# Optimization experiments

Measured on AMD Instinct MI355X. Metric: run time of the kernel, lower is better.

## Reference

```python
import jax, jax.numpy as jnp
import numpy as np

N_NODES = 20000
N_EDGES = 640000
D = 128            # node feature dim
NUM_HEADS = 4      # = num_irreps of edge_sh (lmax=3, 0e+1o+2e+3o)
HEAD_DIM = D // NUM_HEADS
IR_DIMS = np.array([1, 3, 5, 7])  # dims of each irrep; sum = 16
AVG_NUM_NEIGHBORS = 32.0


def setup_inputs() -> dict:
    key = jax.random.key(0)
    ks = jax.random.split(key, 20)
    inp = {
        "edge_sh": jax.random.normal(ks[0], (N_EDGES, int(IR_DIMS.sum())), jnp.float32),
        "node_feats": jax.random.normal(ks[1], (N_NODES, D), jnp.float32),
        "edge_feats": jax.random.normal(ks[2], (N_EDGES, 64), jnp.float32),
        "chi_scalar": jax.random.normal(ks[3], (N_EDGES, 64), jnp.float32),
        "cutoffs": jax.random.uniform(ks[4], (N_EDGES,), jnp.float32),
        "senders": jax.random.randint(ks[5], (N_EDGES,), 0, N_NODES),
        "receivers": jax.random.randint(ks[6], (N_EDGES,), 0, N_NODES),
        # radial MLP: 64 -> 128 -> 128 (silu between)
        "W_rad1": jax.random.normal(ks[7], (64, 128), jnp.float32) / np.sqrt(64),
        "b_rad1": jnp.zeros((128,), jnp.float32),
        "W_rad2": jax.random.normal(ks[8], (128, 128), jnp.float32) / np.sqrt(128),
        "b_rad2": jnp.zeros((128,), jnp.float32),
        # spherical-scalar MLP: 64 -> 128 -> 128
        "W_sph1": jax.random.normal(ks[9], (64, 128), jnp.float32) / np.sqrt(64),
        "b_sph1": jnp.zeros((128,), jnp.float32),
        "W_sph2": jax.random.normal(ks[10], (128, 128), jnp.float32) / np.sqrt(128),
        "b_sph2": jnp.zeros((128,), jnp.float32),
        # Q/K projections, no bias
        "Wq": jax.random.normal(ks[11], (D, D), jnp.float32) / np.sqrt(D),
        "Wk": jax.random.normal(ks[12], (D, D), jnp.float32) / np.sqrt(D),
    }
    return inp


def reference(edge_sh, node_feats, edge_feats, chi_scalar, cutoffs, senders,
              receivers, W_rad1, b_rad1, W_rad2, b_rad2, W_sph1, b_sph1,
              W_sph2, b_sph2, Wq, Wk):
    silu = jax.nn.silu
    # edge filter: radial MLP + spherical-scalar MLP
    w = silu(edge_feats @ W_rad1 + b_rad1) @ W_rad2 + b_rad2      # [E, D]
    w = w + (silu(chi_scalar @ W_sph1 + b_sph1) @ W_sph2 + b_sph2)
    w = w.reshape(-1, NUM_HEADS, HEAD_DIM)                        # [E, H, hd]
    # gathered queries/keys
    q = (node_feats @ Wq).reshape(-1, NUM_HEADS, HEAD_DIM)[receivers]
    k = (node_feats @ Wk).reshape(-1, NUM_HEADS, HEAD_DIM)[senders]
    # filter-scaled attention: per-edge, per-head scalar
    alpha = (q * w * k).sum(axis=-1) * (1.0 / np.sqrt(HEAD_DIM))  # [E, H]
    alpha = alpha * cutoffs[:, None]
    # aligned_mul: broadcast per-irrep weight over each irrep's dim (mul=1)
    y = jnp.repeat(alpha, IR_DIMS, axis=-1)                       # [E, 16]
    msg = edge_sh * y
    # scatter_sum into receivers
    chi = jax.ops.segment_sum(msg, receivers, num_segments=N_NODES)
    return chi / AVG_NUM_NEIGHBORS
```

## Files before the change

### kernel.cpp

```cpp
#include <hip/hip_runtime.h>
#include <cmath>

#define NNODES 20000
#define NEDGES 640000
#define DDIM   128
#define TN     16
#define BE     64

typedef __attribute__((ext_vector_type(8))) short bf16x8;
typedef __attribute__((ext_vector_type(4))) float f32x4;

__device__ __forceinline__ unsigned short f2bf(float x) {
    union { float f; unsigned u; } v; v.f = x;
    unsigned r = v.u + 0x7FFFu + ((v.u >> 16) & 1u);
    return (unsigned short)(r >> 16);
}

__device__ __forceinline__ unsigned cvtpk(float lo, float hi) {
    unsigned r;
    asm("v_cvt_pk_bf16_f32 %0, %1, %2" : "=v"(r) : "v"(lo), "v"(hi));
    return r;
}

__global__ void pack_weights(const float* __restrict__ W, unsigned short* __restrict__ dst)
{
    const int f  = blockIdx.x;
    const int kt = f >> 3, nt = f & 7;
    const int t  = threadIdx.x;
#pragma unroll
    for (int ii = 0; ii < 2; ii++) {
        const int idx  = t * 2 + ii;
        const int lane = idx >> 3, i = idx & 7;
        const int k = kt * 32 + (lane >> 4) * 8 + i;
        const int n = nt * 16 + (lane & 15);
        dst[f * 512 + idx] = f2bf(W[k * 128 + n]);
    }
}

__global__ __launch_bounds__(256) void qk_proj_kernel(
    const float* __restrict__ nf, const float* __restrict__ Wq,
    const float* __restrict__ Wk, float* __restrict__ qbuf,
    float* __restrict__ kbuf)
{
    __shared__ float s_nf[TN * DDIM];
    const int t  = threadIdx.x;
    const int n0 = blockIdx.x * TN;
    {
        const float4* src = (const float4*)(nf + (size_t)n0 * DDIM);
        float4* dst = (float4*)s_nf;
        for (int i = t; i < TN * DDIM / 4; i += 256) dst[i] = src[i];
    }
    __syncthreads();

    const int j = t & 127;
    const float* W = (t < 128) ? Wq : Wk;
    float acc[TN];
#pragma unroll
    for (int n = 0; n < TN; n++) acc[n] = 0.f;

    for (int k = 0; k < DDIM; k += 4) {
        const float w0 = W[(k + 0) * DDIM + j];
        const float w1 = W[(k + 1) * DDIM + j];
        const float w2 = W[(k + 2) * DDIM + j];
        const float w3 = W[(k + 3) * DDIM + j];
#pragma unroll
        for (int n = 0; n < TN; n++) {
            const float4 f = *(const float4*)&s_nf[n * DDIM + k];
            acc[n] = fmaf(f.w, w3, fmaf(f.z, w2, fmaf(f.y, w1, fmaf(f.x, w0, acc[n]))));
        }
    }
    float* outp = (t < 128) ? qbuf : kbuf;
    for (int n = 0; n < TN; n++) outp[(size_t)(n0 + n) * DDIM + j] = acc[n];
}

__global__ __launch_bounds__(256, 3) void edge_kernel(
    const float* __restrict__ edge_sh, const float* __restrict__ cutoffs,
    const int* __restrict__ senders, const int* __restrict__ receivers,
    const float* __restrict__ edge_feats, const float* __restrict__ chi_scalar,
    const unsigned short* __restrict__ w1r, const unsigned short* __restrict__ w1s,
    const unsigned short* __restrict__ w2r, const unsigned short* __restrict__ w2s,
    const float* __restrict__ b_rad1, const float* __restrict__ b_sph1,
    const float* __restrict__ b_rad2, const float* __restrict__ b_sph2,
    const float* __restrict__ qbuf, const float* __restrict__ kbuf,
    float* __restrict__ out)
{
    __shared__ unsigned short s_a[2 * 64 * 64];
    __shared__ unsigned short s_h[64 * 128];
    __shared__ float s_alpha[64][4];
    char* pa = (char*)s_a;
    char* ph = (char*)s_h;

    const int t  = threadIdx.x;
    const int w  = t >> 6;
    const int l  = t & 63;
    const int eb = blockIdx.x * BE;

    const int el     = l & 15;
    const int c0base = w * 32 + (l >> 4) * 4;
    f32x4 qk[2][4];
    float cut[4];
#pragma unroll
    for (int et = 0; et < 4; et++) {
        const int eg = eb + et * 16 + el;
        const int rn = receivers[eg];
        const int sn = senders[eg];
        cut[et] = cutoffs[eg];
#pragma unroll
        for (int ct = 0; ct < 2; ct++) {
            const int c0 = c0base + ct * 16;
            const float4 qv = *(const float4*)(qbuf + (size_t)rn * 128 + c0);
            const float4 kv = *(const float4*)(kbuf + (size_t)sn * 128 + c0);
            qk[ct][et] = (f32x4){ qv.x * kv.x, qv.y * kv.y, qv.z * kv.z, qv.w * kv.w };
        }
    }
    f32x4 b2s[2];
#pragma unroll
    for (int ct = 0; ct < 2; ct++) {
        const float4 br = *(const float4*)(b_rad2 + c0base + ct * 16);
        const float4 bs = *(const float4*)(b_sph2 + c0base + ct * 16);
        b2s[ct] = (f32x4){ br.x + bs.x, br.y + bs.y, br.z + bs.z, br.w + bs.w };
    }
#pragma unroll
    for (int ct = 0; ct < 2; ct++) {
#pragma unroll
        for (int et = 0; et < 4; et++)
            asm volatile("" : "+v"(qk[ct][et]));
        asm volatile("" : "+v"(b2s[ct]));
    }

#pragma unroll
    for (int ii = 0; ii < 4; ii++) {
        const int idx = t + ii * 256;
        const int r   = idx >> 4;
        const int c4  = idx & 15;
        const float4 a = *(const float4*)(edge_feats + (size_t)(eb + r) * 64 + c4 * 4);
        const float4 b = *(const float4*)(chi_scalar + (size_t)(eb + r) * 64 + c4 * 4);
        const uint2 av = { cvtpk(a.x, a.y), cvtpk(a.z, a.w) };
        const uint2 bv = { cvtpk(b.x, b.y), cvtpk(b.z, b.w) };
        const int off = (r * 128 + c4 * 8) ^ ((r & 7) << 4);
        *(uint2*)(pa + off)        = av;
        *(uint2*)(pa + 8192 + off) = bv;
    }
    __syncthreads();

    f32x4 acc2[2][4];
#pragma unroll
    for (int ct = 0; ct < 2; ct++)
#pragma unroll
        for (int et = 0; et < 4; et++)
            acc2[ct][et] = (f32x4){0.f, 0.f, 0.f, 0.f};

    for (int path = 0; path < 2; path++) {
        const unsigned short* W1p = path ? w1s : w1r;
        const unsigned short* W2p = path ? w2s : w2r;
        const float* b1p = path ? b_sph1 : b_rad1;
        const char*  ab  = pa + path * 8192;

        f32x4 acc1[2][4];
#pragma unroll
        for (int ht = 0; ht < 2; ht++)
#pragma unroll
            for (int et = 0; et < 4; et++)
                acc1[ht][et] = (f32x4){0.f, 0.f, 0.f, 0.f};

#pragma unroll
        for (int kt = 0; kt < 2; kt++) {
            bf16x8 bfrag[4];
#pragma unroll
            for (int et = 0; et < 4; et++) {
                const int e = et * 16 + (l & 15);
                const int k = kt * 32 + (l >> 4) * 8;
                bfrag[et] = *(const bf16x8*)(ab + ((e * 128 + k * 2) ^ ((e & 7) << 4)));
            }
#pragma unroll
            for (int ht = 0; ht < 2; ht++) {
                const int f = kt * 8 + (w * 2 + ht);
                const bf16x8 afrag = *(const bf16x8*)(W1p + (size_t)f * 512 + l * 8);
#pragma unroll
                for (int et = 0; et < 4; et++)
                    acc1[ht][et] = __builtin_amdgcn_mfma_f32_16x16x32_bf16(
                        afrag, bfrag[et], acc1[ht][et], 0, 0, 0);
            }
        }

#pragma unroll
        for (int ht = 0; ht < 2; ht++) {
            const int hid0 = w * 32 + ht * 16 + (l >> 4) * 4;
            const float4 bv = *(const float4*)(b1p + hid0);
            const float* bvf = (const float*)&bv;
#pragma unroll
            for (int et = 0; et < 4; et++) {
                const int e = et * 16 + (l & 15);
                float s[4];
#pragma unroll
                for (int r = 0; r < 4; r++) {
                    const float v = acc1[ht][et][r] + bvf[r];
                    s[r] = v * __builtin_amdgcn_rcpf(1.0f + __expf(-v));
                }
                const uint2 hv = { cvtpk(s[0], s[1]), cvtpk(s[2], s[3]) };
                *(uint2*)(ph + ((e * 256 + hid0 * 2) ^ ((e & 7) << 4))) = hv;
            }
        }
        __syncthreads();

#pragma unroll
        for (int kt = 0; kt < 4; kt++) {
            bf16x8 hfrag[4];
#pragma unroll
            for (int et = 0; et < 4; et++) {
                const int e = et * 16 + (l & 15);
                const int k = kt * 32 + (l >> 4) * 8;
                hfrag[et] = *(const bf16x8*)(ph + ((e * 256 + k * 2) ^ ((e & 7) << 4)));
            }
#pragma unroll
            for (int ct = 0; ct < 2; ct++) {
                const int f = kt * 8 + (w * 2 + ct);
                const bf16x8 afrag = *(const bf16x8*)(W2p + (size_t)f * 512 + l * 8);
#pragma unroll
                for (int et = 0; et < 4; et++)
                    acc2[ct][et] = __builtin_amdgcn_mfma_f32_16x16x32_bf16(
                        afrag, hfrag[et], acc2[ct][et], 0, 0, 0);
            }
        }
        if (path == 0) __syncthreads();
    }

#pragma unroll
    for (int et = 0; et < 4; et++) {
        float vsum = 0.f;
#pragma unroll
        for (int ct = 0; ct < 2; ct++) {
#pragma unroll
            for (int r = 0; r < 4; r++)
                vsum = fmaf(qk[ct][et][r], acc2[ct][et][r] + b2s[ct][r], vsum);
        }
        vsum += __shfl_xor(vsum, 16, 64);
        vsum += __shfl_xor(vsum, 32, 64);
        if (l < 16) {
            s_alpha[et * 16 + l][w] = vsum * cut[et] * 0.005524271728019903f;
        }
    }
    __syncthreads();

    {
        const int e   = t >> 2;
        const int c0q = t & 3;
        const int eg  = eb + e;
        const int rn  = receivers[eg];
        const float4 sh = *(const float4*)(edge_sh + (size_t)eg * 16 + c0q * 4);
        const float* shf = (const float*)&sh;
#pragma unroll
        for (int j = 0; j < 4; j++) {
            const int comp = c0q * 4 + j;
            const int head = (comp == 0) ? 0 : (comp < 4) ? 1 : (comp < 9) ? 2 : 3;
            atomicAdd(&out[(size_t)rn * 16 + comp], shf[j] * s_alpha[e][head]);
        }
    }
}

extern "C" void kernel_launch(void* const* d_in, const int* in_sizes, int n_in,
                              void* d_out, int out_size, void* d_ws, size_t ws_size,
                              hipStream_t stream)
{
    const float* edge_sh    = (const float*)d_in[0];
    const float* node_feats = (const float*)d_in[1];
    const float* edge_feats = (const float*)d_in[2];
    const float* chi_scalar = (const float*)d_in[3];
    const float* cutoffs    = (const float*)d_in[4];
    const int*   senders    = (const int*)d_in[5];
    const int*   receivers  = (const int*)d_in[6];
    const float* W_rad1 = (const float*)d_in[7];
    const float* b_rad1 = (const float*)d_in[8];
    const float* W_rad2 = (const float*)d_in[9];
    const float* b_rad2 = (const float*)d_in[10];
    const float* W_sph1 = (const float*)d_in[11];
    const float* b_sph1 = (const float*)d_in[12];
    const float* W_sph2 = (const float*)d_in[13];
    const float* b_sph2 = (const float*)d_in[14];
    const float* Wq     = (const float*)d_in[15];
    const float* Wk     = (const float*)d_in[16];

    float* out  = (float*)d_out;
    float* qbuf = (float*)d_ws;
    float* kbuf = qbuf + (size_t)NNODES * DDIM;
    unsigned short* w1r = (unsigned short*)(kbuf + (size_t)NNODES * DDIM);
    unsigned short* w1s = w1r + 16 * 512;
    unsigned short* w2r = w1s + 16 * 512;
    unsigned short* w2s = w2r + 32 * 512;

    hipMemsetAsync(out, 0, (size_t)out_size * sizeof(float), stream);

    pack_weights<<<16, 256, 0, stream>>>(W_rad1, w1r);
    pack_weights<<<16, 256, 0, stream>>>(W_sph1, w1s);
    pack_weights<<<32, 256, 0, stream>>>(W_rad2, w2r);
    pack_weights<<<32, 256, 0, stream>>>(W_sph2, w2s);

    qk_proj_kernel<<<NNODES / TN, 256, 0, stream>>>(node_feats, Wq, Wk, qbuf, kbuf);

    edge_kernel<<<NEDGES / BE, 256, 0, stream>>>(
        edge_sh, cutoffs, senders, receivers, edge_feats, chi_scalar,
        w1r, w1s, w2r, w2s, b_rad1, b_sph1, b_rad2, b_sph2,
        qbuf, kbuf, out);
}
```

Baseline: 360.7 us.

## Make edge kernel persistent with software-pipelined prefetch of next tile

Converts the edge kernel into a persistent grid of 512 blocks that loop over edge tiles. While the current tile's MLP runs, it prefetches the next tile's indices, q/k gathers and edge/chi features into registers, hiding global-memory latency behind the MFMA work. Occupancy drops to 2 blocks per CU, and register pressure rises because of the prefetch buffers. Barriers are replaced with a custom lgkmcnt wait plus s_barrier.

```diff
diff --git a/kernel.cpp b/kernel.cpp
--- a/kernel.cpp
+++ b/kernel.cpp
@@ -6,6 +6,8 @@
 #define DDIM   128
 #define TN     16
 #define BE     64
+#define NTILES (NEDGES / BE)
+#define NBLK   512
 
 typedef __attribute__((ext_vector_type(8))) short bf16x8;
 typedef __attribute__((ext_vector_type(4))) float f32x4;
@@ -15,11 +17,13 @@
     unsigned r = v.u + 0x7FFFu + ((v.u >> 16) & 1u);
     return (unsigned short)(r >> 16);
 }
-
 __device__ __forceinline__ unsigned cvtpk(float lo, float hi) {
     unsigned r;
     asm("v_cvt_pk_bf16_f32 %0, %1, %2" : "=v"(r) : "v"(lo), "v"(hi));
     return r;
+}
+__device__ __forceinline__ void BAR() {
+    asm volatile("s_waitcnt lgkmcnt(0)\n\ts_barrier" ::: "memory");
 }
 
 __global__ void pack_weights(const float* __restrict__ W, unsigned short* __restrict__ dst)
@@ -73,7 +77,7 @@
     for (int n = 0; n < TN; n++) outp[(size_t)(n0 + n) * DDIM + j] = acc[n];
 }
 
-__global__ __launch_bounds__(256, 3) void edge_kernel(
+__global__ __launch_bounds__(256, 2) void edge_kernel(
     const float* __restrict__ edge_sh, const float* __restrict__ cutoffs,
     const int* __restrict__ senders, const int* __restrict__ receivers,
     const float* __restrict__ edge_feats, const float* __restrict__ chi_scalar,
@@ -93,26 +97,11 @@
     const int t  = threadIdx.x;
     const int w  = t >> 6;
     const int l  = t & 63;
-    const int eb = blockIdx.x * BE;
-
-    const int el     = l & 15;
+    const int el = l & 15;
     const int c0base = w * 32 + (l >> 4) * 4;
-    f32x4 qk[2][4];
-    float cut[4];
-#pragma unroll
-    for (int et = 0; et < 4; et++) {
-        const int eg = eb + et * 16 + el;
-        const int rn = receivers[eg];
-        const int sn = senders[eg];
-        cut[et] = cutoffs[eg];
-#pragma unroll
-        for (int ct = 0; ct < 2; ct++) {
-            const int c0 = c0base + ct * 16;
-            const float4 qv = *(const float4*)(qbuf + (size_t)rn * 128 + c0);
-            const float4 kv = *(const float4*)(kbuf + (size_t)sn * 128 + c0);
-            qk[ct][et] = (f32x4){ qv.x * kv.x, qv.y * kv.y, qv.z * kv.z, qv.w * kv.w };
-        }
-    }
+
+    int tile = blockIdx.x;
+
     f32x4 b2s[2];
 #pragma unroll
     for (int ct = 0; ct < 2; ct++) {
@@ -120,141 +109,226 @@
         const float4 bs = *(const float4*)(b_sph2 + c0base + ct * 16);
         b2s[ct] = (f32x4){ br.x + bs.x, br.y + bs.y, br.z + bs.z, br.w + bs.w };
     }
-#pragma unroll
-    for (int ct = 0; ct < 2; ct++) {
+    float4 b1v[2][2];
+#pragma unroll
+    for (int ht = 0; ht < 2; ht++) {
+        const int hid0 = w * 32 + ht * 16 + (l >> 4) * 4;
+        b1v[0][ht] = *(const float4*)(b_rad1 + hid0);
+        b1v[1][ht] = *(const float4*)(b_sph1 + hid0);
+    }
+
+    float cutC[4], cutN[4], cutP[4];
+    int rnN[4], snN[4];
+    f32x4 qraw[2][4], kraw[2][4];
+    {
+        int rn0[4], sn0[4];
+#pragma unroll
+        for (int et = 0; et < 4; et++) {
+            const int eg = tile * BE + et * 16 + el;
+            rn0[et] = receivers[eg]; sn0[et] = senders[eg]; cutC[et] = cutoffs[eg];
+        }
 #pragma unroll
         for (int et = 0; et < 4; et++)
-            asm volatile("" : "+v"(qk[ct][et]));
-        asm volatile("" : "+v"(b2s[ct]));
-    }
-
-#pragma unroll
-    for (int ii = 0; ii < 4; ii++) {
-        const int idx = t + ii * 256;
-        const int r   = idx >> 4;
-        const int c4  = idx & 15;
-        const float4 a = *(const float4*)(edge_feats + (size_t)(eb + r) * 64 + c4 * 4);
-        const float4 b = *(const float4*)(chi_scalar + (size_t)(eb + r) * 64 + c4 * 4);
-        const uint2 av = { cvtpk(a.x, a.y), cvtpk(a.z, a.w) };
-        const uint2 bv = { cvtpk(b.x, b.y), cvtpk(b.z, b.w) };
-        const int off = (r * 128 + c4 * 8) ^ ((r & 7) << 4);
-        *(uint2*)(pa + off)        = av;
-        *(uint2*)(pa + 8192 + off) = bv;
-    }
-    __syncthreads();
-
-    f32x4 acc2[2][4];
+#pragma unroll
+            for (int ct = 0; ct < 2; ct++) {
+                const float4 qv = *(const float4*)(qbuf + (size_t)rn0[et] * 128 + c0base + ct * 16);
+                const float4 kv = *(const float4*)(kbuf + (size_t)sn0[et] * 128 + c0base + ct * 16);
+                qraw[ct][et] = (f32x4){ qv.x, qv.y, qv.z, qv.w };
+                kraw[ct][et] = (f32x4){ kv.x, kv.y, kv.z, kv.w };
+            }
+        if (tile + NBLK < NTILES) {
+#pragma unroll
+            for (int et = 0; et < 4; et++) {
+                const int eg = (tile + NBLK) * BE + et * 16 + el;
+                rnN[et] = receivers[eg]; snN[et] = senders[eg]; cutN[et] = cutoffs[eg];
+            }
+        }
+#pragma unroll
+        for (int ii = 0; ii < 4; ii++) {
+            const int idx = t + ii * 256;
+            const int r = idx >> 4, c4 = idx & 15;
+            const float4 a = *(const float4*)(edge_feats + (size_t)(tile * BE + r) * 64 + c4 * 4);
+            const float4 b = *(const float4*)(chi_scalar + (size_t)(tile * BE + r) * 64 + c4 * 4);
+            const uint2 av = { cvtpk(a.x, a.y), cvtpk(a.z, a.w) };
+            const uint2 bv = { cvtpk(b.x, b.y), cvtpk(b.z, b.w) };
+            const int off = (r * 128 + c4 * 8) ^ ((r & 7) << 4);
+            *(uint2*)(pa + off)        = av;
+            *(uint2*)(pa + 8192 + off) = bv;
+        }
+        BAR();
+    }
+    f32x4 prod[2][4];
 #pragma unroll
     for (int ct = 0; ct < 2; ct++)
 #pragma unroll
         for (int et = 0; et < 4; et++)
-            acc2[ct][et] = (f32x4){0.f, 0.f, 0.f, 0.f};
-
-    for (int path = 0; path < 2; path++) {
-        const unsigned short* W1p = path ? w1s : w1r;
-        const unsigned short* W2p = path ? w2s : w2r;
-        const float* b1p = path ? b_sph1 : b_rad1;
-        const char*  ab  = pa + path * 8192;
-
-        f32x4 acc1[2][4];
-#pragma unroll
-        for (int ht = 0; ht < 2; ht++)
+            prod[ct][et] = qraw[ct][et] * kraw[ct][et];
+
+    float4 efr[4], chr[4];
+
+    for (;;) {
+        const int next = tile + NBLK;
+        const bool have_next = (next < NTILES);
+
+        if (have_next) {
 #pragma unroll
             for (int et = 0; et < 4; et++)
-                acc1[ht][et] = (f32x4){0.f, 0.f, 0.f, 0.f};
-
-#pragma unroll
-        for (int kt = 0; kt < 2; kt++) {
-            bf16x8 bfrag[4];
+#pragma unroll
+                for (int ct = 0; ct < 2; ct++) {
+                    const float4 qv = *(const float4*)(qbuf + (size_t)rnN[et] * 128 + c0base + ct * 16);
+                    const float4 kv = *(const float4*)(kbuf + (size_t)snN[et] * 128 + c0base + ct * 16);
+                    qraw[ct][et] = (f32x4){ qv.x, qv.y, qv.z, qv.w };
+                    kraw[ct][et] = (f32x4){ kv.x, kv.y, kv.z, kv.w };
+                }
+        }
+#pragma unroll
+        for (int et = 0; et < 4; et++) cutP[et] = cutN[et];
+        if (next + NBLK < NTILES) {
 #pragma unroll
             for (int et = 0; et < 4; et++) {
-                const int e = et * 16 + (l & 15);
-                const int k = kt * 32 + (l >> 4) * 8;
-                bfrag[et] = *(const bf16x8*)(ab + ((e * 128 + k * 2) ^ ((e & 7) << 4)));
-            }
+                const int eg = (next + NBLK) * BE + et * 16 + el;
+                rnN[et] = receivers[eg]; snN[et] = senders[eg]; cutN[et] = cutoffs[eg];
+            }
+        }
+        const int se = tile * BE + (t >> 2);
+        const int rvS = receivers[se];
+        const float4 shS = *(const float4*)(edge_sh + (size_t)se * 16 + (t & 3) * 4);
+
+        f32x4 acc2[2][4];
+#pragma unroll
+        for (int ct = 0; ct < 2; ct++)
+#pragma unroll
+            for (int et = 0; et < 4; et++)
+                acc2[ct][et] = (f32x4){0.f, 0.f, 0.f, 0.f};
+
+#pragma unroll
+        for (int path = 0; path < 2; path++) {
+            const unsigned short* W1p = path ? w1s : w1r;
+            const unsigned short* W2p = path ? w2s : w2r;
+            const char* ab = pa + path * 8192;
+
+            f32x4 acc1[2][4];
+#pragma unroll
+            for (int ht = 0; ht < 2; ht++)
+#pragma unroll
+                for (int et = 0; et < 4; et++)
+                    acc1[ht][et] = (f32x4){0.f, 0.f, 0.f, 0.f};
+
+#pragma unroll
+            for (int kt = 0; kt < 2; kt++) {
+                bf16x8 bfrag[4];
+#pragma unroll
+                for (int et = 0; et < 4; et++) {
+                    const int e = et * 16 + el;
+                    const int k = kt * 32 + (l >> 4) * 8;
+                    bfrag[et] = *(const bf16x8*)(ab + ((e * 128 + k * 2) ^ ((e & 7) << 4)));
+                }
+#pragma unroll
+                for (int ht = 0; ht < 2; ht++) {
+                    const bf16x8 afrag = *(const bf16x8*)(W1p + (size_t)(kt * 8 + w * 2 + ht) * 512 + l * 8);
+#pragma unroll
+                    for (int et = 0; et < 4; et++)
+                        acc1[ht][et] = __builtin_amdgcn_mfma_f32_16x16x32_bf16(
+                            afrag, bfrag[et], acc1[ht][et], 0, 0, 0);
+                }
+            }
+
 #pragma unroll
             for (int ht = 0; ht < 2; ht++) {
-                const int f = kt * 8 + (w * 2 + ht);
-                const bf16x8 afrag = *(const bf16x8*)(W1p + (size_t)f * 512 + l * 8);
-#pragma unroll
-                for (int et = 0; et < 4; et++)
-                    acc1[ht][et] = __builtin_amdgcn_mfma_f32_16x16x32_bf16(
-                        afrag, bfrag[et], acc1[ht][et], 0, 0, 0);
-            }
-        }
-
-#pragma unroll
-        for (int ht = 0; ht < 2; ht++) {
-            const int hid0 = w * 32 + ht * 16 + (l >> 4) * 4;
-            const float4 bv = *(const float4*)(b1p + hid0);
-            const float* bvf = (const float*)&bv;
-#pragma unroll
-            for (int et = 0; et < 4; et++) {
-                const int e = et * 16 + (l & 15);
-                float s[4];
-#pragma unroll
-                for (int r = 0; r < 4; r++) {
-                    const float v = acc1[ht][et][r] + bvf[r];
-                    s[r] = v * __builtin_amdgcn_rcpf(1.0f + __expf(-v));
-                }
-                const uint2 hv = { cvtpk(s[0], s[1]), cvtpk(s[2], s[3]) };
-                *(uint2*)(ph + ((e * 256 + hid0 * 2) ^ ((e & 7) << 4))) = hv;
-            }
-        }
-        __syncthreads();
-
-#pragma unroll
-        for (int kt = 0; kt < 4; kt++) {
-            bf16x8 hfrag[4];
-#pragma unroll
-            for (int et = 0; et < 4; et++) {
-                const int e = et * 16 + (l & 15);
-                const int k = kt * 32 + (l >> 4) * 8;
-                hfrag[et] = *(const bf16x8*)(ph + ((e * 256 + k * 2) ^ ((e & 7) << 4)));
-            }
-#pragma unroll
-            for (int ct = 0; ct < 2; ct++) {
-                const int f = kt * 8 + (w * 2 + ct);
-                const bf16x8 afrag = *(const bf16x8*)(W2p + (size_t)f * 512 + l * 8);
-#pragma unroll
-                for (int et = 0; et < 4; et++)
-                    acc2[ct][et] = __builtin_amdgcn_mfma_f32_16x16x32_bf16(
-                        afrag, hfrag[et], acc2[ct][et], 0, 0, 0);
-            }
-        }
-        if (path == 0) __syncthreads();
-    }
-
-#pragma unroll
-    for (int et = 0; et < 4; et++) {
-        float vsum = 0.f;
-#pragma unroll
-        for (int ct = 0; ct < 2; ct++) {
-#pragma unroll
-            for (int r = 0; r < 4; r++)
-                vsum = fmaf(qk[ct][et][r], acc2[ct][et][r] + b2s[ct][r], vsum);
-        }
-        vsum += __shfl_xor(vsum, 16, 64);
-        vsum += __shfl_xor(vsum, 32, 64);
-        if (l < 16) {
-            s_alpha[et * 16 + l][w] = vsum * cut[et] * 0.005524271728019903f;
-        }
-    }
-    __syncthreads();
-
-    {
-        const int e   = t >> 2;
-        const int c0q = t & 3;
-        const int eg  = eb + e;
-        const int rn  = receivers[eg];
-        const float4 sh = *(const float4*)(edge_sh + (size_t)eg * 16 + c0q * 4);
-        const float* shf = (const float*)&sh;
-#pragma unroll
-        for (int j = 0; j < 4; j++) {
-            const int comp = c0q * 4 + j;
-            const int head = (comp == 0) ? 0 : (comp < 4) ? 1 : (comp < 9) ? 2 : 3;
-            atomicAdd(&out[(size_t)rn * 16 + comp], shf[j] * s_alpha[e][head]);
-        }
+                const int hid0 = w * 32 + ht * 16 + (l >> 4) * 4;
+                const float* bvf = (const float*)&b1v[path][ht];
+#pragma unroll
+                for (int et = 0; et < 4; et++) {
+                    const int e = et * 16 + el;
+                    float s[4];
+#pragma unroll
+                    for (int r = 0; r < 4; r++) {
+                        const float v = acc1[ht][et][r] + bvf[r];
+                        s[r] = v * __builtin_amdgcn_rcpf(1.0f + __expf(-v));
+                    }
+                    const uint2 hv = { cvtpk(s[0], s[1]), cvtpk(s[2], s[3]) };
+                    *(uint2*)(ph + ((e * 256 + hid0 * 2) ^ ((e & 7) << 4))) = hv;
+                }
+            }
+            BAR();
+
+#pragma unroll
+            for (int kt = 0; kt < 4; kt++) {
+                bf16x8 hfrag[4];
+#pragma unroll
+                for (int et = 0; et < 4; et++) {
+                    const int e = et * 16 + el;
+                    const int k = kt * 32 + (l >> 4) * 8;
+                    hfrag[et] = *(const bf16x8*)(ph + ((e * 256 + k * 2) ^ ((e & 7) << 4)));
+                }
+#pragma unroll
+                for (int ct = 0; ct < 2; ct++) {
+                    const bf16x8 afrag = *(const bf16x8*)(W2p + (size_t)(kt * 8 + w * 2 + ct) * 512 + l * 8);
+#pragma unroll
+                    for (int et = 0; et < 4; et++)
+                        acc2[ct][et] = __builtin_amdgcn_mfma_f32_16x16x32_bf16(
+                            afrag, hfrag[et], acc2[ct][et], 0, 0, 0);
+                }
+            }
+            if (path == 0) BAR();
+        }
+
+        if (have_next) {
+#pragma unroll
+            for (int ii = 0; ii < 4; ii++) {
+                const int idx = t + ii * 256;
+                const int r = idx >> 4, c4 = idx & 15;
+                efr[ii] = *(const float4*)(edge_feats + (size_t)(next * BE + r) * 64 + c4 * 4);
+                chr[ii] = *(const float4*)(chi_scalar + (size_t)(next * BE + r) * 64 + c4 * 4);
+            }
+        }
+#pragma unroll
+        for (int et = 0; et < 4; et++) {
+            float vsum = 0.f;
+#pragma unroll
+            for (int ct = 0; ct < 2; ct++)
+#pragma unroll
+                for (int r = 0; r < 4; r++)
+                    vsum = fmaf(prod[ct][et][r], acc2[ct][et][r] + b2s[ct][r], vsum);
+            vsum += __shfl_xor(vsum, 16, 64);
+            vsum += __shfl_xor(vsum, 32, 64);
+            if (l < 16) {
+                s_alpha[et * 16 + l][w] = vsum * cutC[et] * 0.005524271728019903f;
+            }
+        }
+        BAR();
+
+        {
+            const float* shf = (const float*)&shS;
+#pragma unroll
+            for (int j = 0; j < 4; j++) {
+                const int comp = (t & 3) * 4 + j;
+                const int head = (comp == 0) ? 0 : (comp < 4) ? 1 : (comp < 9) ? 2 : 3;
+                atomicAdd(&out[(size_t)rvS * 16 + comp], shf[j] * s_alpha[t >> 2][head]);
+            }
+        }
+
+        if (!have_next) break;
+
+#pragma unroll
+        for (int ct = 0; ct < 2; ct++)
+#pragma unroll
+            for (int et = 0; et < 4; et++)
+                prod[ct][et] = qraw[ct][et] * kraw[ct][et];
+#pragma unroll
+        for (int ii = 0; ii < 4; ii++) {
+            const int idx = t + ii * 256;
+            const int r = idx >> 4, c4 = idx & 15;
+            const uint2 av = { cvtpk(efr[ii].x, efr[ii].y), cvtpk(efr[ii].z, efr[ii].w) };
+            const uint2 bv = { cvtpk(chr[ii].x, chr[ii].y), cvtpk(chr[ii].z, chr[ii].w) };
+            const int off = (r * 128 + c4 * 8) ^ ((r & 7) << 4);
+            *(uint2*)(pa + off)        = av;
+            *(uint2*)(pa + 8192 + off) = bv;
+        }
+#pragma unroll
+        for (int et = 0; et < 4; et++) cutC[et] = cutP[et];
+        BAR();
+        tile = next;
     }
 }
 
@@ -297,7 +371,7 @@
 
     qk_proj_kernel<<<NNODES / TN, 256, 0, stream>>>(node_feats, Wq, Wk, qbuf, kbuf);
 
-    edge_kernel<<<NEDGES / BE, 256, 0, stream>>>(
+    edge_kernel<<<NBLK, 256, 0, stream>>>(
         edge_sh, cutoffs, senders, receivers, edge_feats, chi_scalar,
         w1r, w1s, w2r, w2s, b_rad1, b_sph1, b_rad2, b_sph2,
         qbuf, kbuf, out);
```

Result: slower. 712.8 us (+97.6%).

## Store Q/K in bf16 and stage q*k products in LDS instead of registers

Applied to the files above, without the earlier changes.

The Q/K projection now writes bf16 instead of fp32, which halves the bytes the edge kernel gathers per edge. The edge kernel computes q*k products with coalesced row-wise gathers, stores them as bf16 in a swizzled shared buffer, and reads them back after the MLP GEMMs rather than keeping them in registers. The launch-bounds occupancy hint is dropped and the path loop is unrolled. The change adds 16KB of LDS per block and extra rounding of q, k and their product to bf16, which lowers precision.

```diff
diff --git a/kernel.cpp b/kernel.cpp
--- a/kernel.cpp
+++ b/kernel.cpp
@@ -9,13 +9,16 @@
 
 typedef __attribute__((ext_vector_type(8))) short bf16x8;
 typedef __attribute__((ext_vector_type(4))) float f32x4;
+typedef __attribute__((ext_vector_type(4))) unsigned short us4;
 
 __device__ __forceinline__ unsigned short f2bf(float x) {
     union { float f; unsigned u; } v; v.f = x;
     unsigned r = v.u + 0x7FFFu + ((v.u >> 16) & 1u);
     return (unsigned short)(r >> 16);
 }
-
+__device__ __forceinline__ float bf2f(unsigned short h) {
+    union { unsigned u; float f; } v; v.u = ((unsigned)h) << 16; return v.f;
+}
 __device__ __forceinline__ unsigned cvtpk(float lo, float hi) {
     unsigned r;
     asm("v_cvt_pk_bf16_f32 %0, %1, %2" : "=v"(r) : "v"(lo), "v"(hi));
@@ -39,8 +42,8 @@
 
 __global__ __launch_bounds__(256) void qk_proj_kernel(
     const float* __restrict__ nf, const float* __restrict__ Wq,
-    const float* __restrict__ Wk, float* __restrict__ qbuf,
-    float* __restrict__ kbuf)
+    const float* __restrict__ Wk, unsigned short* __restrict__ qbuf,
+    unsigned short* __restrict__ kbuf)
 {
     __shared__ float s_nf[TN * DDIM];
     const int t  = threadIdx.x;
@@ -69,11 +72,11 @@
             acc[n] = fmaf(f.w, w3, fmaf(f.z, w2, fmaf(f.y, w1, fmaf(f.x, w0, acc[n]))));
         }
     }
-    float* outp = (t < 128) ? qbuf : kbuf;
-    for (int n = 0; n < TN; n++) outp[(size_t)(n0 + n) * DDIM + j] = acc[n];
-}
-
-__global__ __launch_bounds__(256, 3) void edge_kernel(
+    unsigned short* outp = (t < 128) ? qbuf : kbuf;
+    for (int n = 0; n < TN; n++) outp[(size_t)(n0 + n) * DDIM + j] = f2bf(acc[n]);
+}
+
+__global__ __launch_bounds__(256) void edge_kernel(
     const float* __restrict__ edge_sh, const float* __restrict__ cutoffs,
     const int* __restrict__ senders, const int* __restrict__ receivers,
     const float* __restrict__ edge_feats, const float* __restrict__ chi_scalar,
@@ -81,51 +84,38 @@
     const unsigned short* __restrict__ w2r, const unsigned short* __restrict__ w2s,
     const float* __restrict__ b_rad1, const float* __restrict__ b_sph1,
     const float* __restrict__ b_rad2, const float* __restrict__ b_sph2,
-    const float* __restrict__ qbuf, const float* __restrict__ kbuf,
+    const unsigned short* __restrict__ qbuf, const unsigned short* __restrict__ kbuf,
     float* __restrict__ out)
 {
     __shared__ unsigned short s_a[2 * 64 * 64];
     __shared__ unsigned short s_h[64 * 128];
+    __shared__ unsigned short s_p[64 * 128];
     __shared__ float s_alpha[64][4];
+
     char* pa = (char*)s_a;
     char* ph = (char*)s_h;
+    char* pp = (char*)s_p;
 
     const int t  = threadIdx.x;
     const int w  = t >> 6;
     const int l  = t & 63;
     const int eb = blockIdx.x * BE;
 
-    const int el     = l & 15;
-    const int c0base = w * 32 + (l >> 4) * 4;
-    f32x4 qk[2][4];
-    float cut[4];
-#pragma unroll
-    for (int et = 0; et < 4; et++) {
-        const int eg = eb + et * 16 + el;
-        const int rn = receivers[eg];
-        const int sn = senders[eg];
-        cut[et] = cutoffs[eg];
-#pragma unroll
-        for (int ct = 0; ct < 2; ct++) {
-            const int c0 = c0base + ct * 16;
-            const float4 qv = *(const float4*)(qbuf + (size_t)rn * 128 + c0);
-            const float4 kv = *(const float4*)(kbuf + (size_t)sn * 128 + c0);
-            qk[ct][et] = (f32x4){ qv.x * kv.x, qv.y * kv.y, qv.z * kv.z, qv.w * kv.w };
-        }
-    }
-    f32x4 b2s[2];
-#pragma unroll
-    for (int ct = 0; ct < 2; ct++) {
-        const float4 br = *(const float4*)(b_rad2 + c0base + ct * 16);
-        const float4 bs = *(const float4*)(b_sph2 + c0base + ct * 16);
-        b2s[ct] = (f32x4){ br.x + bs.x, br.y + bs.y, br.z + bs.z, br.w + bs.w };
-    }
-#pragma unroll
-    for (int ct = 0; ct < 2; ct++) {
-#pragma unroll
-        for (int et = 0; et < 4; et++)
-            asm volatile("" : "+v"(qk[ct][et]));
-        asm volatile("" : "+v"(b2s[ct]));
+#pragma unroll
+    for (int ii = 0; ii < 8; ii++) {
+        const int e  = w * 16 + ii * 2 + (l >> 5);
+        const int eg = eb + e;
+        const int r  = receivers[eg];
+        const int s  = senders[eg];
+        const int c4 = l & 31;
+        const us4 qv = *(const us4*)(qbuf + (size_t)r * 128 + c4 * 4);
+        const us4 kv = *(const us4*)(kbuf + (size_t)s * 128 + c4 * 4);
+        const float p0 = bf2f(qv[0]) * bf2f(kv[0]);
+        const float p1 = bf2f(qv[1]) * bf2f(kv[1]);
+        const float p2 = bf2f(qv[2]) * bf2f(kv[2]);
+        const float p3 = bf2f(qv[3]) * bf2f(kv[3]);
+        const uint2 pv = { cvtpk(p0, p1), cvtpk(p2, p3) };
+        *(uint2*)(pp + ((e * 256 + c4 * 8) ^ ((e & 7) << 4))) = pv;
     }
 
 #pragma unroll
@@ -150,6 +140,7 @@
         for (int et = 0; et < 4; et++)
             acc2[ct][et] = (f32x4){0.f, 0.f, 0.f, 0.f};
 
+#pragma unroll
     for (int path = 0; path < 2; path++) {
         const unsigned short* W1p = path ? w1s : w1r;
         const unsigned short* W2p = path ? w2s : w2r;
@@ -225,19 +216,33 @@
         if (path == 0) __syncthreads();
     }
 
-#pragma unroll
-    for (int et = 0; et < 4; et++) {
-        float vsum = 0.f;
+    {
+        f32x4 b2s[2];
 #pragma unroll
         for (int ct = 0; ct < 2; ct++) {
-#pragma unroll
-            for (int r = 0; r < 4; r++)
-                vsum = fmaf(qk[ct][et][r], acc2[ct][et][r] + b2s[ct][r], vsum);
-        }
-        vsum += __shfl_xor(vsum, 16, 64);
-        vsum += __shfl_xor(vsum, 32, 64);
-        if (l < 16) {
-            s_alpha[et * 16 + l][w] = vsum * cut[et] * 0.005524271728019903f;
+            const int c0 = w * 32 + ct * 16 + (l >> 4) * 4;
+            const float4 br = *(const float4*)(b_rad2 + c0);
+            const float4 bs = *(const float4*)(b_sph2 + c0);
+            b2s[ct] = (f32x4){ br.x + bs.x, br.y + bs.y, br.z + bs.z, br.w + bs.w };
+        }
+#pragma unroll
+        for (int et = 0; et < 4; et++) {
+            const int e = et * 16 + (l & 15);
+            float vsum = 0.f;
+#pragma unroll
+            for (int ct = 0; ct < 2; ct++) {
+                const int c0 = w * 32 + ct * 16 + (l >> 4) * 4;
+                const us4 pv = *(const us4*)(pp + ((e * 256 + c0 * 2) ^ ((e & 7) << 4)));
+#pragma unroll
+                for (int r = 0; r < 4; r++)
+                    vsum = fmaf(bf2f(pv[r]), acc2[ct][et][r] + b2s[ct][r], vsum);
+            }
+            vsum += __shfl_xor(vsum, 16, 64);
+            vsum += __shfl_xor(vsum, 32, 64);
+            if (l < 16) {
+                s_alpha[et * 16 + l][w] = vsum * cutoffs[eb + et * 16 + l]
+                                        * 0.005524271728019903f;
+            }
         }
     }
     __syncthreads();
@@ -280,13 +285,13 @@
     const float* Wq     = (const float*)d_in[15];
     const float* Wk     = (const float*)d_in[16];
 
-    float* out  = (float*)d_out;
-    float* qbuf = (float*)d_ws;
-    float* kbuf = qbuf + (size_t)NNODES * DDIM;
-    unsigned short* w1r = (unsigned short*)(kbuf + (size_t)NNODES * DDIM);
-    unsigned short* w1s = w1r + 16 * 512;
-    unsigned short* w2r = w1s + 16 * 512;
-    unsigned short* w2s = w2r + 32 * 512;
+    float* out = (float*)d_out;
+    unsigned short* qbuf = (unsigned short*)d_ws;
+    unsigned short* kbuf = qbuf + (size_t)NNODES * DDIM;
+    unsigned short* w1r  = kbuf + (size_t)NNODES * DDIM;
+    unsigned short* w1s  = w1r + 16 * 512;
+    unsigned short* w2r  = w1s + 16 * 512;
+    unsigned short* w2s  = w2r + 32 * 512;
 
     hipMemsetAsync(out, 0, (size_t)out_size * sizeof(float), stream);
 
```

Measured after the change: 290.3 us. -19.5%, faster.
